# Kernel tuning notes

Measured on AMD Instinct MI355X. Metric: run time of the kernel, lower is better.

## Reference

```python
import jax, jax.numpy as jnp
import numpy as np

N_NODES = 100_000
N_EDGES = 3_200_000
N_ELEMS = 10

# ase.data.covalent_radii (Cordero 2008), missing = 0.2, padded to 119 entries
_COV = [0.2, 0.31, 0.28, 1.28, 0.96, 0.84, 0.76, 0.71, 0.66, 0.57, 0.58, 1.66,
        1.41, 1.21, 1.11, 1.07, 1.05, 1.02, 1.06, 2.03, 1.76, 1.70, 1.60, 1.53,
        1.39, 1.39, 1.32, 1.26, 1.24, 1.32, 1.22, 1.22, 1.20, 1.19, 1.20, 1.20,
        1.16, 2.20, 1.95, 1.90, 1.75, 1.64, 1.54, 1.47, 1.46, 1.42, 1.39, 1.45,
        1.44, 1.42, 1.39, 1.39, 1.38, 1.39, 1.40, 2.44, 2.15, 2.07, 2.04, 2.03,
        2.01, 1.99, 1.98, 1.98, 1.96, 1.94, 1.92, 1.92, 1.89, 1.90, 1.87, 1.87,
        1.75, 1.70, 1.62, 1.51, 1.44, 1.41, 1.36, 1.36, 1.32, 1.45, 1.46, 1.48,
        1.40, 1.50, 1.50, 2.60, 2.21, 2.15, 2.06, 2.00, 1.96, 1.90, 1.87, 1.80,
        1.69] + [0.2] * 22
COVALENT_RADII = jnp.asarray(np.array(_COV, dtype=np.float32))
C = jnp.asarray(np.array([0.1818, 0.5099, 0.2802, 0.02817], dtype=np.float32))
P = 6.0          # polynomial cutoff order
A_EXP = 0.3
A_PREF = 0.4543


def setup_inputs() -> dict:
    key = jax.random.key(0)
    k1, k2, k3, k4 = jax.random.split(key, 4)
    # per-edge distances in a physically plausible range (strictly > 0)
    x = jax.random.uniform(k1, (N_EDGES, 1), dtype=jnp.float32, minval=0.5, maxval=4.5)
    edge_index = jax.random.randint(k2, (2, N_EDGES), 0, N_NODES)
    # one-hot node element attributes
    elem_idx = jax.random.randint(k3, (N_NODES,), 0, N_ELEMS)
    node_attrs = jax.nn.one_hot(elem_idx, N_ELEMS, dtype=jnp.float32)
    # atomic number per element type, in [1, 90)
    atomic_numbers = jax.random.randint(k4, (N_ELEMS,), 1, 90)
    return {"x": x, "node_attrs": node_attrs, "edge_index": edge_index,
            "atomic_numbers": atomic_numbers}


def _poly_envelope(x, r_max, p):
    r = x / r_max
    env = (1.0 - (p + 1.0) * (p + 2.0) / 2.0 * jnp.power(r, p)
           + p * (p + 2.0) * jnp.power(r, p + 1.0)
           - p * (p + 1.0) / 2.0 * jnp.power(r, p + 2.0))
    return env * (x < r_max)


def reference(x, node_attrs, edge_index, atomic_numbers):
    sender, receiver = edge_index[0], edge_index[1]
    # gather per-node atomic numbers via one-hot argmax, then per-edge
    node_Z = atomic_numbers[jnp.argmax(node_attrs, axis=1)][:, None]  # [N,1]
    Z_u = node_Z[sender].astype(jnp.int32)  # [E,1]
    Z_v = node_Z[receiver].astype(jnp.int32)  # [E,1]
    Zu_f = Z_u.astype(x.dtype)
    Zv_f = Z_v.astype(x.dtype)
    a = A_PREF * 0.529 / (jnp.power(Zu_f, A_EXP) + jnp.power(Zv_f, A_EXP))
    r_over_a = x / a
    phi = (C[0] * jnp.exp(-3.2 * r_over_a) + C[1] * jnp.exp(-0.9423 * r_over_a)
           + C[2] * jnp.exp(-0.4028 * r_over_a) + C[3] * jnp.exp(-0.2016 * r_over_a))
    v_edges = 14.3996 * Zu_f * Zv_f / x * phi  # [E,1]
    r_max = (COVALENT_RADII[Z_u] + COVALENT_RADII[Z_v]).astype(x.dtype)  # [E,1]
    v_edges = 0.5 * v_edges * _poly_envelope(x, r_max, jnp.asarray(P, x.dtype))
    V_ZBL = jax.ops.segment_sum(v_edges, receiver, num_segments=node_attrs.shape[0])
    return jnp.squeeze(V_ZBL, axis=-1)  # [N]
```

## Files before the change

### kernel.cpp

```cpp
#include <hip/hip_runtime.h>

#define NELEMS 10
#define W_SHIFT 10
#define W 1024
#define MAXBL 128
#define CHUNK 4096
#define EPT 8
#define BS 512
#define PAD 4
#define SLABCAP (CHUNK + MAXBL * (PAD - 1))
#define PKCAP 50176
#define INV_A_PREF (1.0f / (0.4543f * 0.529f))

__constant__ float c_cov[119] = {
    0.2f, 0.31f, 0.28f, 1.28f, 0.96f, 0.84f, 0.76f, 0.71f, 0.66f, 0.57f, 0.58f, 1.66f,
    1.41f, 1.21f, 1.11f, 1.07f, 1.05f, 1.02f, 1.06f, 2.03f, 1.76f, 1.70f, 1.60f, 1.53f,
    1.39f, 1.39f, 1.32f, 1.26f, 1.24f, 1.32f, 1.22f, 1.22f, 1.20f, 1.19f, 1.20f, 1.20f,
    1.16f, 2.20f, 1.95f, 1.90f, 1.75f, 1.64f, 1.54f, 1.47f, 1.46f, 1.42f, 1.39f, 1.45f,
    1.44f, 1.42f, 1.39f, 1.39f, 1.38f, 1.39f, 1.40f, 2.44f, 2.15f, 2.07f, 2.04f, 2.03f,
    2.01f, 1.99f, 1.98f, 1.98f, 1.96f, 1.94f, 1.92f, 1.92f, 1.89f, 1.90f, 1.87f, 1.87f,
    1.75f, 1.70f, 1.62f, 1.51f, 1.44f, 1.41f, 1.36f, 1.36f, 1.32f, 1.45f, 1.46f, 1.48f,
    1.40f, 1.50f, 1.50f, 2.60f, 2.21f, 2.15f, 2.06f, 2.00f, 1.96f, 1.90f, 1.87f, 1.80f,
    1.69f,
    0.2f, 0.2f, 0.2f, 0.2f, 0.2f, 0.2f, 0.2f, 0.2f, 0.2f, 0.2f, 0.2f,
    0.2f, 0.2f, 0.2f, 0.2f, 0.2f, 0.2f, 0.2f, 0.2f, 0.2f, 0.2f, 0.2f
};

__global__ __launch_bounds__(256)
void zbl_node_elem(const float* __restrict__ node_attrs,
                   const int* __restrict__ atomic_numbers,
                   unsigned char* __restrict__ elem,
                   unsigned char* __restrict__ packed,
                   float4* __restrict__ etab_g, int n_nodes) {
    __shared__ float rows[256 * NELEMS];
    __shared__ unsigned char earr[256];
    int t = threadIdx.x;
    if (blockIdx.x == 0 && t < NELEMS) {
        int Z = atomic_numbers[t];
        float zf = (float)Z;
        etab_g[t] = make_float4(zf, powf(zf, 0.3f), c_cov[Z], 0.0f);
    }
    int n0 = blockIdx.x * 256;
    int nrow = min(256, n_nodes - n0);
    int nflt = nrow * NELEMS;
    const float* src = node_attrs + (size_t)n0 * NELEMS;
    for (int i = t; i < nflt; i += 256) rows[i] = src[i];
    __syncthreads();
    if (t < nrow) {
        const float* a = rows + t * NELEMS;
        int best = 0;
        float bv = a[0];
#pragma unroll
        for (int k = 1; k < NELEMS; ++k) {
            float v = a[k];
            if (v > bv) { bv = v; best = k; }
        }
        earr[t] = (unsigned char)best;
        elem[n0 + t] = (unsigned char)best;
    }
    __syncthreads();
    if (t < 128 && 2 * t < nrow) {
        unsigned char lo = earr[2 * t];
        unsigned char hi = (2 * t + 1 < nrow) ? earr[2 * t + 1] : 0;
        packed[(n0 >> 1) + t] = (unsigned char)(lo | (hi << 4));
    }
}

__device__ __forceinline__ float zbl_edge_value_p(float xv, float A, float B,
                                                  float C) {
    float roa = xv * B;
    float phi = 0.1818f  * __expf(-3.2f    * roa)
              + 0.5099f  * __expf(-0.9423f * roa)
              + 0.2802f  * __expf(-0.4028f * roa)
              + 0.02817f * __expf(-0.2016f * roa);
    float v = A / xv * phi;
    float rr = xv / C;
    float rr2 = rr * rr;
    float rr3 = rr2 * rr;
    float rr6 = rr3 * rr3;
    float rr7 = rr6 * rr;
    float rr8 = rr7 * rr;
    float env = 1.0f - 28.0f * rr6 + 48.0f * rr7 - 21.0f * rr8;
    env = (xv < C) ? env : 0.0f;
    return 0.5f * v * env;
}

__global__ __launch_bounds__(BS)
void zbl_fused(const float* __restrict__ x,
               const int* __restrict__ ei,
               const unsigned char* __restrict__ packed,
               const float4* __restrict__ etab_g,
               int n_edges, int n_nodes, int nb, int slab,
               float* __restrict__ valg,
               unsigned short* __restrict__ lrg,
               int* __restrict__ offg ) {
    __shared__ unsigned char  pk[PKCAP];
    __shared__ float          val_s[SLABCAP];
    __shared__ unsigned short lr_s[SLABCAP];
    __shared__ int   lds_off[MAXBL + 1];
    __shared__ int   cursor[MAXBL];
    __shared__ float ptabA[NELEMS * NELEMS];
    __shared__ float ptabB[NELEMS * NELEMS];
    __shared__ float ptabC[NELEMS * NELEMS];

    int blk = blockIdx.x;
    int t = threadIdx.x;
    int e0 = blk * CHUNK;
    int e1 = min(n_edges, e0 + CHUNK);
    const int* send = ei;
    const int* recv = ei + n_edges;
    bool full = (e0 + CHUNK <= n_edges);

    if (t < MAXBL) cursor[t] = 0;
    __syncthreads();

    {
        const unsigned int* ps = (const unsigned int*)packed;
        unsigned int* pd = (unsigned int*)pk;
        int npk = (n_nodes + 1) >> 1;
        int nw = npk >> 2;
        for (int i = t; i < nw; i += BS) pd[i] = ps[i];
        for (int i = (nw << 2) + t; i < npk; i += BS) pk[i] = packed[i];
    }
    for (int i = t; i < (SLABCAP >> 2); i += BS) {
        ((float4*)val_s)[i] = make_float4(0.f, 0.f, 0.f, 0.f);
        ((uint2*)lr_s)[i]   = make_uint2(0u, 0u);
    }
    if (t < NELEMS * NELEMS) {
        float4 u = etab_g[t / NELEMS];
        float4 v = etab_g[t % NELEMS];
        ptabA[t] = 14.3996f * u.x * v.x;
        ptabB[t] = (u.y + v.y) * INV_A_PREF;
        ptabC[t] = u.z + v.z;
    }

    int rv[EPT], sv[EPT];
    float xv[EPT];
    if (full) {
        const int4*   rp = (const int4*)(recv + e0);
        const int4*   sp = (const int4*)(send + e0);
        const float4* xp = (const float4*)(x + e0);
        int4 ra = rp[2 * t], rb = rp[2 * t + 1];
        int4 sa = sp[2 * t], sb = sp[2 * t + 1];
        float4 xa = xp[2 * t], xb = xp[2 * t + 1];
        rv[0] = ra.x; rv[1] = ra.y; rv[2] = ra.z; rv[3] = ra.w;
        rv[4] = rb.x; rv[5] = rb.y; rv[6] = rb.z; rv[7] = rb.w;
        sv[0] = sa.x; sv[1] = sa.y; sv[2] = sa.z; sv[3] = sa.w;
        sv[4] = sb.x; sv[5] = sb.y; sv[6] = sb.z; sv[7] = sb.w;
        xv[0] = xa.x; xv[1] = xa.y; xv[2] = xa.z; xv[3] = xa.w;
        xv[4] = xb.x; xv[5] = xb.y; xv[6] = xb.z; xv[7] = xb.w;
#pragma unroll
        for (int i = 0; i < EPT; ++i)
            atomicAdd(&cursor[rv[i] >> W_SHIFT], 1);
    } else {
        for (int e = e0 + t; e < e1; e += BS)
            atomicAdd(&cursor[recv[e] >> W_SHIFT], 1);
    }
    __syncthreads();

    if (t < 64) {
        int a = (t < nb)      ? ((cursor[t]      + (PAD - 1)) & ~(PAD - 1)) : 0;
        int b = (t + 64 < nb) ? ((cursor[t + 64] + (PAD - 1)) & ~(PAD - 1)) : 0;
        int a0 = a, b0 = b;
#pragma unroll
        for (int d = 1; d < 64; d <<= 1) {
            int va = __shfl_up(a, d);
            int vb = __shfl_up(b, d);
            if (t >= d) { a += va; b += vb; }
        }
        int totA = __shfl(a, 63);
        b += totA;
        lds_off[t + 1]  = a;
        lds_off[t + 65] = b;
        cursor[t]       = a - a0;
        cursor[t + 64]  = b - b0;
        if (t == 0) lds_off[0] = 0;
    }
    __syncthreads();

    int total = lds_off[nb];

    if (full) {
#pragma unroll
        for (int i = 0; i < EPT; ++i) {
            int s = sv[i], r = rv[i];
            int es = (pk[s >> 1] >> ((s & 1) << 2)) & 15;
            int er = (pk[r >> 1] >> ((r & 1) << 2)) & 15;
            int pi = es * NELEMS + er;
            float v = zbl_edge_value_p(xv[i], ptabA[pi], ptabB[pi], ptabC[pi]);
            int pos = atomicAdd(&cursor[r >> W_SHIFT], 1);
            val_s[pos] = v;
            lr_s[pos] = (unsigned short)(r & (W - 1));
        }
    } else {
        for (int e = e0 + t; e < e1; e += BS) {
            int s = send[e], r = recv[e];
            int es = (pk[s >> 1] >> ((s & 1) << 2)) & 15;
            int er = (pk[r >> 1] >> ((r & 1) << 2)) & 15;
            int pi = es * NELEMS + er;
            float v = zbl_edge_value_p(x[e], ptabA[pi], ptabB[pi], ptabC[pi]);
            int pos = atomicAdd(&cursor[r >> W_SHIFT], 1);
            val_s[pos] = v;
            lr_s[pos] = (unsigned short)(r & (W - 1));
        }
    }
    __syncthreads();

    size_t gb = (size_t)blk * slab;
    float4* vdst = (float4*)(valg + gb);
    uint2*  ldst = (uint2*)(lrg + gb);
    int nt4 = total >> 2;
    for (int i = t; i < nt4; i += BS) {
        vdst[i] = ((float4*)val_s)[i];
        ldst[i] = ((uint2*)lr_s)[i];
    }
    if (t <= nb) offg[blk * (nb + 1) + t] = lds_off[t];
}

__global__ __launch_bounds__(BS)
void zbl_reduce_seg(const float* __restrict__ valg,
                    const unsigned short* __restrict__ lrg,
                    const int* __restrict__ offg,
                    int nblk, int nb, int kred, int slab,
                    float* __restrict__ partial) {
    __shared__ float acc[W];
    int b = blockIdx.x;
    int j = blockIdx.y;
    int t = threadIdx.x;
    acc[t] = 0.0f;
    acc[t + BS] = 0.0f;
    __syncthreads();

    int stride = (nblk + kred - 1) / kred;
    int blk0 = j * stride;
    int blk1 = min(nblk, blk0 + stride);
    int wave = t >> 6, lane = t & 63;
    int sw = lane >> 4, li = lane & 15;
    const int NSW = (BS / 64) * 4;

    for (int blk = blk0 + wave * 4 + sw; blk < blk1; blk += NSW) {
        const int* po = offg + (size_t)blk * (nb + 1) + b;
        int s0 = po[0], s1 = po[1];
        size_t gb = (size_t)blk * slab;
        const float4*  v4 = (const float4*)(valg + gb);
        const ushort4* l4 = (const ushort4*)(lrg + gb);
        for (int q = (s0 >> 2) + li; q < (s1 >> 2); q += 16) {
            float4  v = v4[q];
            ushort4 l = l4[q];
            atomicAdd(&acc[l.x], v.x);
            atomicAdd(&acc[l.y], v.y);
            atomicAdd(&acc[l.z], v.z);
            atomicAdd(&acc[l.w], v.w);
        }
    }
    __syncthreads();
    float* dst = partial + (((size_t)b * kred + j) << W_SHIFT);
    dst[t] = acc[t];
    dst[t + BS] = acc[t + BS];
}

__global__ void zbl_combine(const float* __restrict__ partial, int kred,
                            int n_nodes, float* __restrict__ out) {
    int q = blockIdx.x * blockDim.x + threadIdx.x;
    int n = q << 2;
    if (n >= n_nodes) return;
    int b = n >> W_SHIFT;
    int t = n & (W - 1);
    float4 s = make_float4(0.f, 0.f, 0.f, 0.f);
    for (int j = 0; j < kred; ++j) {
        const float4* p =
            (const float4*)(partial + (((size_t)b * kred + j) << W_SHIFT) + t);
        float4 v = *p;
        s.x += v.x; s.y += v.y; s.z += v.z; s.w += v.w;
    }
    if (n + 3 < n_nodes) {
        *(float4*)(out + n) = s;
    } else {
        out[n] = s.x;
        if (n + 1 < n_nodes) out[n + 1] = s.y;
        if (n + 2 < n_nodes) out[n + 2] = s.z;
    }
}

__global__ void zbl_edge_atomic(const float* __restrict__ x,
                                const int* __restrict__ edge_index,
                                const unsigned char* __restrict__ elem,
                                const float4* __restrict__ etab_g,
                                float* __restrict__ out, int n_edges) {
    int e = blockIdx.x * blockDim.x + threadIdx.x;
    if (e >= n_edges) return;
    int s = edge_index[e];
    int r = edge_index[n_edges + e];
    float4 u = etab_g[elem[s]];
    float4 w = etab_g[elem[r]];
    float v = zbl_edge_value_p(x[e], 14.3996f * u.x * w.x,
                               (u.y + w.y) * INV_A_PREF, u.z + w.z);
#if defined(__HIP_PLATFORM_AMD__)
    unsafeAtomicAdd(out + r, v);
#else
    atomicAdd(out + r, v);
#endif
}

extern "C" void kernel_launch(void* const* d_in, const int* in_sizes, int n_in,
                              void* d_out, int out_size, void* d_ws, size_t ws_size,
                              hipStream_t stream) {
    const float* x              = (const float*)d_in[0];
    const float* node_attrs     = (const float*)d_in[1];
    const int*   edge_index     = (const int*)d_in[2];
    const int*   atomic_numbers = (const int*)d_in[3];
    float*       out            = (float*)d_out;

    int n_edges = in_sizes[0];
    int n_nodes = in_sizes[1] / NELEMS;
    int nb = (n_nodes + W - 1) / W;
    int nblk = (n_edges + CHUNK - 1) / CHUNK;
    int slab = (CHUNK + nb * (PAD - 1) + 3) & ~3;

    char* ws = (char*)d_ws;

    int kred = 0;
    size_t elem_o = 0, pk_o = 0, etab_o = 0,
           val_o = 0, lr_o = 0, offg_o = 0, part_o = 0;
    for (int try_k = 16; try_k >= 1; try_k >>= 1) {
        size_t off = 0;
        auto alloc = [&](size_t bytes) {
            size_t o = off;
            off = (off + bytes + 255) & ~(size_t)255;
            return o;
        };
        elem_o = alloc((size_t)n_nodes);
        pk_o   = alloc((size_t)(n_nodes + 1) / 2);
        etab_o = alloc(NELEMS * sizeof(float4));
        val_o  = alloc((size_t)nblk * slab * sizeof(float));
        lr_o   = alloc((size_t)nblk * slab * sizeof(unsigned short));
        offg_o = alloc((size_t)nblk * (nb + 1) * sizeof(int));
        part_o = alloc((size_t)nb * try_k * W * sizeof(float));
        if (off <= ws_size) { kred = try_k; break; }
    }

    unsigned char* elem   = (unsigned char*)(ws + elem_o);
    unsigned char* packed = (unsigned char*)(ws + pk_o);
    float4* etab_g        = (float4*)(ws + etab_o);

    int nb_nodes = (n_nodes + 255) / 256;
    zbl_node_elem<<<nb_nodes, 256, 0, stream>>>(node_attrs, atomic_numbers,
                                                elem, packed, etab_g, n_nodes);

    bool fast_ok = (kred >= 1) && (nb <= MAXBL) && (slab <= SLABCAP) &&
                   (((n_nodes + 1) >> 1) <= PKCAP);

    if (fast_ok) {
        float* valg         = (float*)(ws + val_o);
        unsigned short* lrg = (unsigned short*)(ws + lr_o);
        int* offg           = (int*)(ws + offg_o);
        float* partial      = (float*)(ws + part_o);

        zbl_fused<<<nblk, BS, 0, stream>>>(x, edge_index, packed, etab_g,
                                           n_edges, n_nodes, nb, slab,
                                           valg, lrg, offg);
        zbl_reduce_seg<<<dim3(nb, kred), BS, 0, stream>>>(valg, lrg, offg, nblk,
                                                          nb, kred, slab, partial);
        int nq = (n_nodes + 3) >> 2;
        zbl_combine<<<(nq + 255) / 256, 256, 0, stream>>>(partial, kred,
                                                          n_nodes, out);
    } else {
        hipMemsetAsync(d_out, 0, (size_t)out_size * sizeof(float), stream);
        int nb_edges = (n_edges + 255) / 256;
        zbl_edge_atomic<<<nb_edges, 256, 0, stream>>>(x, edge_index, elem, etab_g,
                                                      out, n_edges);
    }
}
```

Measured before the change: 59.25 us.

## Make fused edge kernel persistent with prefetch of the next chunk

The fused edge kernel now runs a grid capped at 512 blocks, and each block loops over several edge chunks. The packed element table (about 50 KB) is copied into LDS once per block instead of once per chunk. While one chunk is being computed and written out, the loads for the next chunk are already issued, and the scan runs concurrently with slab zeroing. The node-attribute staging buffer is padded to stride 11 to avoid LDS bank conflicts, and the reduction split factor is capped at 8 instead of 16. The cost is higher register pressure from the double-buffered registers and fewer resident blocks to hide latency.

```diff
diff --git a/kernel.cpp b/kernel.cpp
--- a/kernel.cpp
+++ b/kernel.cpp
@@ -10,6 +10,7 @@
 #define PAD 4
 #define SLABCAP (CHUNK + MAXBL * (PAD - 1))
 #define PKCAP 50176
+#define GRIDP 512
 #define INV_A_PREF (1.0f / (0.4543f * 0.529f))
 
 __constant__ float c_cov[119] = {
@@ -32,7 +33,7 @@
                    unsigned char* __restrict__ elem,
                    unsigned char* __restrict__ packed,
                    float4* __restrict__ etab_g, int n_nodes) {
-    __shared__ float rows[256 * NELEMS];
+    __shared__ float rows[256 * 11];
     __shared__ unsigned char earr[256];
     int t = threadIdx.x;
     if (blockIdx.x == 0 && t < NELEMS) {
@@ -44,10 +45,13 @@
     int nrow = min(256, n_nodes - n0);
     int nflt = nrow * NELEMS;
     const float* src = node_attrs + (size_t)n0 * NELEMS;
-    for (int i = t; i < nflt; i += 256) rows[i] = src[i];
+    for (int i = t; i < nflt; i += 256) {
+        int rr = i / NELEMS, cc = i - rr * NELEMS;
+        rows[rr * 11 + cc] = src[i];
+    }
     __syncthreads();
     if (t < nrow) {
-        const float* a = rows + t * NELEMS;
+        const float* a = rows + t * 11;
         int best = 0;
         float bv = a[0];
 #pragma unroll
@@ -85,12 +89,52 @@
     return 0.5f * v * env;
 }
 
+#define LOADBURST(c, RV, SV, XV)                                          \
+    do {                                                                  \
+        int _e0 = (c) * CHUNK;                                            \
+        const int4*   _rp = (const int4*)(recv + _e0);                    \
+        const int4*   _sp = (const int4*)(send + _e0);                    \
+        const float4* _xp = (const float4*)(x + _e0);                     \
+        int4 _ra = _rp[2 * t], _rb = _rp[2 * t + 1];                      \
+        int4 _sa = _sp[2 * t], _sb = _sp[2 * t + 1];                      \
+        float4 _xa = _xp[2 * t], _xb = _xp[2 * t + 1];                    \
+        RV[0]=_ra.x; RV[1]=_ra.y; RV[2]=_ra.z; RV[3]=_ra.w;               \
+        RV[4]=_rb.x; RV[5]=_rb.y; RV[6]=_rb.z; RV[7]=_rb.w;               \
+        SV[0]=_sa.x; SV[1]=_sa.y; SV[2]=_sa.z; SV[3]=_sa.w;               \
+        SV[4]=_sb.x; SV[5]=_sb.y; SV[6]=_sb.z; SV[7]=_sb.w;               \
+        XV[0]=_xa.x; XV[1]=_xa.y; XV[2]=_xa.z; XV[3]=_xa.w;               \
+        XV[4]=_xb.x; XV[5]=_xb.y; XV[6]=_xb.z; XV[7]=_xb.w;               \
+    } while (0)
+
+#define SCAN_W0()                                                         \
+    do {                                                                  \
+        if (t < 64) {                                                     \
+            int a = (t < nb)      ? ((cntA[t]      + (PAD-1)) & ~(PAD-1)) : 0; \
+            int b = (t + 64 < nb) ? ((cntA[t + 64] + (PAD-1)) & ~(PAD-1)) : 0; \
+            int a0 = a, b0 = b;                                           \
+            _Pragma("unroll")                                             \
+            for (int d = 1; d < 64; d <<= 1) {                            \
+                int va = __shfl_up(a, d);                                 \
+                int vb = __shfl_up(b, d);                                 \
+                if (t >= d) { a += va; b += vb; }                         \
+            }                                                             \
+            int totA = __shfl(a, 63);                                     \
+            b += totA;                                                    \
+            lds_off[t + 1]  = a;                                          \
+            lds_off[t + 65] = b;                                          \
+            curB[t]       = a - a0;                                       \
+            curB[t + 64]  = b - b0;                                       \
+            cntA[t] = 0; cntA[t + 64] = 0;                                \
+            if (t == 0) lds_off[0] = 0;                                   \
+        }                                                                 \
+    } while (0)
+
 __global__ __launch_bounds__(BS)
 void zbl_fused(const float* __restrict__ x,
                const int* __restrict__ ei,
                const unsigned char* __restrict__ packed,
                const float4* __restrict__ etab_g,
-               int n_edges, int n_nodes, int nb, int slab,
+               int n_edges, int n_nodes, int nb, int slab, int nchunks,
                float* __restrict__ valg,
                unsigned short* __restrict__ lrg,
                int* __restrict__ offg ) {
@@ -98,21 +142,18 @@
     __shared__ float          val_s[SLABCAP];
     __shared__ unsigned short lr_s[SLABCAP];
     __shared__ int   lds_off[MAXBL + 1];
-    __shared__ int   cursor[MAXBL];
+    __shared__ int   curB[MAXBL];
+    __shared__ int   cntA[MAXBL];
     __shared__ float ptabA[NELEMS * NELEMS];
     __shared__ float ptabB[NELEMS * NELEMS];
     __shared__ float ptabC[NELEMS * NELEMS];
 
-    int blk = blockIdx.x;
     int t = threadIdx.x;
-    int e0 = blk * CHUNK;
-    int e1 = min(n_edges, e0 + CHUNK);
     const int* send = ei;
     const int* recv = ei + n_edges;
-    bool full = (e0 + CHUNK <= n_edges);
-
-    if (t < MAXBL) cursor[t] = 0;
-    __syncthreads();
+
+    int c = blockIdx.x;
+    if (c >= nchunks) return;
 
     {
         const unsigned int* ps = (const unsigned int*)packed;
@@ -126,6 +167,7 @@
         ((float4*)val_s)[i] = make_float4(0.f, 0.f, 0.f, 0.f);
         ((uint2*)lr_s)[i]   = make_uint2(0u, 0u);
     }
+    if (t < MAXBL) cntA[t] = 0;
     if (t < NELEMS * NELEMS) {
         float4 u = etab_g[t / NELEMS];
         float4 v = etab_g[t % NELEMS];
@@ -136,85 +178,98 @@
 
     int rv[EPT], sv[EPT];
     float xv[EPT];
-    if (full) {
-        const int4*   rp = (const int4*)(recv + e0);
-        const int4*   sp = (const int4*)(send + e0);
-        const float4* xp = (const float4*)(x + e0);
-        int4 ra = rp[2 * t], rb = rp[2 * t + 1];
-        int4 sa = sp[2 * t], sb = sp[2 * t + 1];
-        float4 xa = xp[2 * t], xb = xp[2 * t + 1];
-        rv[0] = ra.x; rv[1] = ra.y; rv[2] = ra.z; rv[3] = ra.w;
-        rv[4] = rb.x; rv[5] = rb.y; rv[6] = rb.z; rv[7] = rb.w;
-        sv[0] = sa.x; sv[1] = sa.y; sv[2] = sa.z; sv[3] = sa.w;
-        sv[4] = sb.x; sv[5] = sb.y; sv[6] = sb.z; sv[7] = sb.w;
-        xv[0] = xa.x; xv[1] = xa.y; xv[2] = xa.z; xv[3] = xa.w;
-        xv[4] = xb.x; xv[5] = xb.y; xv[6] = xb.z; xv[7] = xb.w;
-#pragma unroll
-        for (int i = 0; i < EPT; ++i)
-            atomicAdd(&cursor[rv[i] >> W_SHIFT], 1);
-    } else {
-        for (int e = e0 + t; e < e1; e += BS)
-            atomicAdd(&cursor[recv[e] >> W_SHIFT], 1);
-    }
-    __syncthreads();
-
-    if (t < 64) {
-        int a = (t < nb)      ? ((cursor[t]      + (PAD - 1)) & ~(PAD - 1)) : 0;
-        int b = (t + 64 < nb) ? ((cursor[t + 64] + (PAD - 1)) & ~(PAD - 1)) : 0;
-        int a0 = a, b0 = b;
-#pragma unroll
-        for (int d = 1; d < 64; d <<= 1) {
-            int va = __shfl_up(a, d);
-            int vb = __shfl_up(b, d);
-            if (t >= d) { a += va; b += vb; }
-        }
-        int totA = __shfl(a, 63);
-        b += totA;
-        lds_off[t + 1]  = a;
-        lds_off[t + 65] = b;
-        cursor[t]       = a - a0;
-        cursor[t + 64]  = b - b0;
-        if (t == 0) lds_off[0] = 0;
-    }
-    __syncthreads();
-
-    int total = lds_off[nb];
+    bool full = (c * CHUNK + CHUNK <= n_edges);
+    if (full) LOADBURST(c, rv, sv, xv);
+    __syncthreads();
 
     if (full) {
 #pragma unroll
+        for (int i = 0; i < EPT; ++i) atomicAdd(&cntA[rv[i] >> W_SHIFT], 1);
+    } else {
+        for (int e = c * CHUNK + t; e < n_edges; e += BS)
+            atomicAdd(&cntA[recv[e] >> W_SHIFT], 1);
+    }
+    __syncthreads();
+    SCAN_W0();
+    __syncthreads();
+
+    while (true) {
+        int n = c + gridDim.x;
+        bool has_next = (n < nchunks);
+        bool nfull = has_next && (n * CHUNK + CHUNK <= n_edges);
+        int rv2[EPT], sv2[EPT];
+        float xv2[EPT];
+        if (nfull) LOADBURST(n, rv2, sv2, xv2);
+
+        if (full) {
+#pragma unroll
+            for (int i = 0; i < EPT; ++i) {
+                int s = sv[i], r = rv[i];
+                int es = (pk[s >> 1] >> ((s & 1) << 2)) & 15;
+                int er = (pk[r >> 1] >> ((r & 1) << 2)) & 15;
+                int pi = es * NELEMS + er;
+                float v = zbl_edge_value_p(xv[i], ptabA[pi], ptabB[pi], ptabC[pi]);
+                int pos = atomicAdd(&curB[r >> W_SHIFT], 1);
+                val_s[pos] = v;
+                lr_s[pos] = (unsigned short)(r & (W - 1));
+            }
+        } else {
+            for (int e = c * CHUNK + t; e < n_edges; e += BS) {
+                int s = send[e], r = recv[e];
+                int es = (pk[s >> 1] >> ((s & 1) << 2)) & 15;
+                int er = (pk[r >> 1] >> ((r & 1) << 2)) & 15;
+                int pi = es * NELEMS + er;
+                float v = zbl_edge_value_p(x[e], ptabA[pi], ptabB[pi], ptabC[pi]);
+                int pos = atomicAdd(&curB[r >> W_SHIFT], 1);
+                val_s[pos] = v;
+                lr_s[pos] = (unsigned short)(r & (W - 1));
+            }
+        }
+        __syncthreads();
+
+        {
+            int total = lds_off[nb];
+            size_t gb = (size_t)c * slab;
+            float4* vdst = (float4*)(valg + gb);
+            uint2*  ldst = (uint2*)(lrg + gb);
+            int nt4 = total >> 2;
+            for (int i = t; i < nt4; i += BS) {
+                vdst[i] = ((float4*)val_s)[i];
+                ldst[i] = ((uint2*)lr_s)[i];
+            }
+            if (t <= nb) offg[c * (nb + 1) + t] = lds_off[t];
+        }
+        if (has_next) {
+            if (nfull) {
+#pragma unroll
+                for (int i = 0; i < EPT; ++i)
+                    atomicAdd(&cntA[rv2[i] >> W_SHIFT], 1);
+            } else {
+                for (int e = n * CHUNK + t; e < n_edges; e += BS)
+                    atomicAdd(&cntA[recv[e] >> W_SHIFT], 1);
+            }
+        }
+        __syncthreads();
+
+        if (!has_next) break;
+
+        if (t >= 64) {
+            for (int i = t - 64; i < (SLABCAP >> 2); i += BS - 64) {
+                ((float4*)val_s)[i] = make_float4(0.f, 0.f, 0.f, 0.f);
+                ((uint2*)lr_s)[i]   = make_uint2(0u, 0u);
+            }
+        } else {
+            SCAN_W0();
+        }
+        __syncthreads();
+
+        c = n;
+        full = nfull;
+#pragma unroll
         for (int i = 0; i < EPT; ++i) {
-            int s = sv[i], r = rv[i];
-            int es = (pk[s >> 1] >> ((s & 1) << 2)) & 15;
-            int er = (pk[r >> 1] >> ((r & 1) << 2)) & 15;
-            int pi = es * NELEMS + er;
-            float v = zbl_edge_value_p(xv[i], ptabA[pi], ptabB[pi], ptabC[pi]);
-            int pos = atomicAdd(&cursor[r >> W_SHIFT], 1);
-            val_s[pos] = v;
-            lr_s[pos] = (unsigned short)(r & (W - 1));
-        }
-    } else {
-        for (int e = e0 + t; e < e1; e += BS) {
-            int s = send[e], r = recv[e];
-            int es = (pk[s >> 1] >> ((s & 1) << 2)) & 15;
-            int er = (pk[r >> 1] >> ((r & 1) << 2)) & 15;
-            int pi = es * NELEMS + er;
-            float v = zbl_edge_value_p(x[e], ptabA[pi], ptabB[pi], ptabC[pi]);
-            int pos = atomicAdd(&cursor[r >> W_SHIFT], 1);
-            val_s[pos] = v;
-            lr_s[pos] = (unsigned short)(r & (W - 1));
-        }
-    }
-    __syncthreads();
-
-    size_t gb = (size_t)blk * slab;
-    float4* vdst = (float4*)(valg + gb);
-    uint2*  ldst = (uint2*)(lrg + gb);
-    int nt4 = total >> 2;
-    for (int i = t; i < nt4; i += BS) {
-        vdst[i] = ((float4*)val_s)[i];
-        ldst[i] = ((uint2*)lr_s)[i];
-    }
-    if (t <= nb) offg[blk * (nb + 1) + t] = lds_off[t];
+            rv[i] = rv2[i]; sv[i] = sv2[i]; xv[i] = xv2[i];
+        }
+    }
 }
 
 __global__ __launch_bounds__(BS)
@@ -322,7 +377,7 @@
     int kred = 0;
     size_t elem_o = 0, pk_o = 0, etab_o = 0,
            val_o = 0, lr_o = 0, offg_o = 0, part_o = 0;
-    for (int try_k = 16; try_k >= 1; try_k >>= 1) {
+    for (int try_k = 8; try_k >= 1; try_k >>= 1) {
         size_t off = 0;
         auto alloc = [&](size_t bytes) {
             size_t o = off;
@@ -356,9 +411,10 @@
         int* offg           = (int*)(ws + offg_o);
         float* partial      = (float*)(ws + part_o);
 
-        zbl_fused<<<nblk, BS, 0, stream>>>(x, edge_index, packed, etab_g,
-                                           n_edges, n_nodes, nb, slab,
-                                           valg, lrg, offg);
+        int gridP = nblk < GRIDP ? nblk : GRIDP;
+        zbl_fused<<<gridP, BS, 0, stream>>>(x, edge_index, packed, etab_g,
+                                            n_edges, n_nodes, nb, slab, nblk,
+                                            valg, lrg, offg);
         zbl_reduce_seg<<<dim3(nb, kred), BS, 0, stream>>>(valg, lrg, offg, nblk,
                                                           nb, kred, slab, partial);
         int nq = (n_nodes + 3) >> 2;
```

New measurement: 57.86 us. 1.02x faster.
